# Optimization experiments

Hardware: AMD Instinct MI355X
Metric: run time of the kernel (lower is better)

The kernel has to match this reference:

```python
import jax, jax.numpy as jnp
import numpy as np


def setup_inputs() -> dict:
    key = jax.random.key(0)
    k1, k2 = jax.random.split(key)
    B, C, H, W = 16, 128, 128, 128
    x = jax.random.normal(k1, (B, C, H, W), dtype=jnp.float32)
    # 1x1 conv weight, no bias: [out_channels, in_channels]
    w = jax.random.normal(k2, (C, C), dtype=jnp.float32) * (1.0 / np.sqrt(C))
    return {"x": x, "w": w}


def reference(x, w):
    # x: [B, C, H, W]; original computes y = x @ (x^T x) / (H*W) over flattened
    # spatial dim N = H*W, then a 1x1 conv. We reassociate exactly:
    #   x @ (x^T x) == (x x^T) @ x   (associativity of matmul)
    # avoiding the O(N^2) intermediate; math is identical.
    B, C, H, W = x.shape
    N = H * W
    xf = x.reshape(B, C, N)                              # [B, C, N]
    gram = jnp.einsum('bcn,bdn->bcd', xf, xf) / N        # [B, C, C] = (x x^T)/N
    y = jnp.einsum('bcd,bdn->bcn', gram, xf)             # [B, C, N]
    y = y.reshape(B, C, H, W)
    # 1x1 conv (bias=False) == per-pixel channel mixing
    out = jnp.einsum('oc,bchw->bohw', w, y)              # [B, C, H, W]
    return out
```

## Files before the change

### kernel.cpp

```cpp
#include <hip/hip_runtime.h>

typedef __attribute__((ext_vector_type(8))) short bf16x8;
typedef __attribute__((ext_vector_type(4))) float f32x4;
typedef __attribute__((ext_vector_type(4))) float f4v;
typedef __attribute__((ext_vector_type(4))) unsigned short u16x4;

#define NB 16
#define NC 128
#define NN 16384
#define CHUNKS 32
#define KSTEPS 8

__device__ __forceinline__ unsigned int f2bf_pack(float lo, float hi) {
  unsigned int ulo = __float_as_uint(lo);
  unsigned int uhi = __float_as_uint(hi);
  ulo = (ulo + 0x7FFFu + ((ulo >> 16) & 1u)) >> 16;
  uhi = (uhi + 0x7FFFu + ((uhi >> 16) & 1u)) & 0xFFFF0000u;
  return ulo | uhi;
}

__device__ __forceinline__ unsigned short f2bf_one(float v) {
  unsigned int u = __float_as_uint(v);
  return (unsigned short)((u + 0x7FFFu + ((u >> 16) & 1u)) >> 16);
}

__device__ __forceinline__ float bf2f(unsigned short u) {
  return __uint_as_float(((unsigned int)u) << 16);
}

__global__ __launch_bounds__(256, 2)
void nlm_gram_kernel(const float* __restrict__ x, unsigned short* __restrict__ partials) {
  __shared__ __align__(16) char lds[2 * 128 * 64 * 2];
  const int t = threadIdx.x;
  const int g = blockIdx.x;
  const int b  = g / CHUNKS;
  const int ch = g % CHUNKS;
  const int lane = t & 63, wv = t >> 6, l15 = lane & 15, q = lane >> 4;

  const float* xb = x + (size_t)b * NC * NN + (size_t)ch * (KSTEPS * 64);

  f32x4 acc[2][8];
#pragma unroll
  for (int i = 0; i < 2; ++i)
#pragma unroll
    for (int j = 0; j < 8; ++j) acc[i][j] = (f32x4){0.f, 0.f, 0.f, 0.f};

  int srow[4], sseg[4];
#pragma unroll
  for (int i = 0; i < 4; ++i) { int id = t + 256 * i; srow[i] = id >> 3; sseg[i] = id & 7; }

  f4v pfA[4][2], pfB[4][2];

#define LOADPF(PF, KS)                                                      \
  {                                                                         \
    _Pragma("unroll") for (int i = 0; i < 4; ++i) {                         \
      const float* src = xb + (size_t)srow[i] * NN + (KS)*64 + sseg[i] * 8; \
      PF[i][0] = *(const f4v*)src;                                          \
      PF[i][1] = *(const f4v*)(src + 4);                                    \
    }                                                                       \
  }

#define PACKPF(PF, BUF)                                                     \
  {                                                                         \
    _Pragma("unroll") for (int i = 0; i < 4; ++i) {                         \
      uint4 pk;                                                             \
      pk.x = f2bf_pack(PF[i][0][0], PF[i][0][1]);                           \
      pk.y = f2bf_pack(PF[i][0][2], PF[i][0][3]);                           \
      pk.z = f2bf_pack(PF[i][1][0], PF[i][1][1]);                           \
      pk.w = f2bf_pack(PF[i][1][2], PF[i][1][3]);                           \
      int byte = (srow[i] * 128 + sseg[i] * 16) ^ ((srow[i] & 7) << 4);     \
      *(uint4*)((BUF) + byte) = pk;                                         \
    }                                                                       \
  }

#define MFMAPH(BUF)                                                                          \
  {                                                                                          \
    _Pragma("unroll") for (int kh = 0; kh < 2; ++kh) {                                       \
      const int kbyte = kh * 64 + q * 16;                                                    \
      int ra = wv * 32 + l15;                                                                \
      bf16x8 a0 = *(const bf16x8*)((BUF) + ((ra * 128 + kbyte) ^ ((ra & 7) << 4)));          \
      int rb = wv * 32 + 16 + l15;                                                           \
      bf16x8 a1 = *(const bf16x8*)((BUF) + ((rb * 128 + kbyte) ^ ((rb & 7) << 4)));          \
      _Pragma("unroll") for (int ct = 0; ct < 8; ++ct) {                                     \
        int rc = ct * 16 + l15;                                                              \
        bf16x8 bb = *(const bf16x8*)((BUF) + ((rc * 128 + kbyte) ^ ((rc & 7) << 4)));        \
        acc[0][ct] = __builtin_amdgcn_mfma_f32_16x16x32_bf16(a0, bb, acc[0][ct], 0, 0, 0);   \
        acc[1][ct] = __builtin_amdgcn_mfma_f32_16x16x32_bf16(a1, bb, acc[1][ct], 0, 0, 0);   \
      }                                                                                      \
    }                                                                                        \
  }

  char* buf0 = lds;
  char* buf1 = lds + 16384;

  LOADPF(pfA, 0);
  PACKPF(pfA, buf0);
  LOADPF(pfB, 1);
  __syncthreads();

#pragma unroll 1
  for (int ks = 0; ks < KSTEPS; ks += 2) {
    if (ks + 2 < KSTEPS) LOADPF(pfA, ks + 2);
    MFMAPH(buf0);
    if (ks + 1 < KSTEPS) PACKPF(pfB, buf1);
    __syncthreads();
    if (ks + 1 < KSTEPS) {
      if (ks + 3 < KSTEPS) LOADPF(pfB, ks + 3);
      MFMAPH(buf1);
      if (ks + 2 < KSTEPS) PACKPF(pfA, buf0);
      __syncthreads();
    }
  }

  unsigned short* lds16 = (unsigned short*)lds;
#pragma unroll
  for (int rt = 0; rt < 2; ++rt)
#pragma unroll
    for (int ct = 0; ct < 8; ++ct)
#pragma unroll
      for (int r = 0; r < 4; ++r) {
        int i = wv * 32 + rt * 16 + q * 4 + r;
        int j = ct * 16 + l15;
        lds16[i * 128 + j] = f2bf_one(acc[rt][ct][r]);
      }
  __syncthreads();

  unsigned short* part = partials + (size_t)g * (NC * NC);
#pragma unroll
  for (int ii = 0; ii < 8; ++ii) {
    int off = ii * 4096 + t * 16;
    *(uint4*)((char*)part + off) = *(const uint4*)(lds + off);
  }
#undef LOADPF
#undef PACKPF
#undef MFMAPH
}

__global__ __launch_bounds__(256)
void nlm_gramw_kernel(const unsigned short* __restrict__ partials, const float* __restrict__ w,
                      unsigned short* __restrict__ Mbf) {
  __shared__ __align__(16) float glds[8 * 128];
  const int t = threadIdx.x;
  const int b  = blockIdx.x >> 4;
  const int d0 = (blockIdx.x & 15) * 8;

  const int rr = t >> 5;
  const int c4 = (t & 31) * 4;
  const unsigned short* pb =
      partials + (size_t)b * CHUNKS * (NC * NC) + (d0 + rr) * 128 + c4;
  f4v s = (f4v){0.f, 0.f, 0.f, 0.f};
  for (int chn = 0; chn < CHUNKS; ++chn) {
    u16x4 v = *(const u16x4*)(pb + (size_t)chn * (NC * NC));
    s[0] += bf2f(v[0]);
    s[1] += bf2f(v[1]);
    s[2] += bf2f(v[2]);
    s[3] += bf2f(v[3]);
  }
  s *= (1.0f / 16384.0f);
  *(f4v*)(glds + rr * 128 + c4) = s;
  __syncthreads();

  const int o  = t & 127;
  const int j0 = (t >> 7) * 4;
  float m[4] = {0.f, 0.f, 0.f, 0.f};
  for (int c = 0; c < 128; c += 4) {
    f4v wr = *(const f4v*)(w + o * 128 + c);
#pragma unroll
    for (int j = 0; j < 4; ++j) {
      f4v gv = *(const f4v*)(glds + (j0 + j) * 128 + c);
      m[j] = fmaf(wr[0], gv[0], m[j]);
      m[j] = fmaf(wr[1], gv[1], m[j]);
      m[j] = fmaf(wr[2], gv[2], m[j]);
      m[j] = fmaf(wr[3], gv[3], m[j]);
    }
  }
  uint2 pk;
  pk.x = f2bf_pack(m[0], m[1]);
  pk.y = f2bf_pack(m[2], m[3]);
  *(uint2*)(Mbf + (size_t)b * NC * NC + o * 128 + d0 + j0) = pk;
}

__global__ __launch_bounds__(256, 2)
void nlm_out_kernel(const float* __restrict__ x, const unsigned short* __restrict__ Mbf,
                    float* __restrict__ out) {
  __shared__ __align__(16) char lds[128 * 128 * 2];
  const int t = threadIdx.x;
  const int b = (NB - 1) - (blockIdx.x >> 7);
  const int n0 = (blockIdx.x & 127) * 128;
  const int lane = t & 63, wv = t >> 6, l15 = lane & 15, q = lane >> 4;

  bf16x8 afr[2][4];
  const unsigned short* mb = Mbf + (size_t)b * NC * NC;
#pragma unroll
  for (int rt = 0; rt < 2; ++rt)
#pragma unroll
    for (int ks = 0; ks < 4; ++ks) {
      int o = wv * 32 + rt * 16 + l15;
      afr[rt][ks] = *(const bf16x8*)(mb + o * 128 + ks * 32 + q * 8);
    }

  const float* xb = x + (size_t)b * NC * NN + n0;
#pragma unroll
  for (int i = 0; i < 2; ++i) {
    int id = t + 256 * i;
    int nb = id & 31, cb = id >> 5;
    const float* src = xb + (size_t)(cb * 8) * NN + nb * 4;
    f4v v[8];
#pragma unroll
    for (int r = 0; r < 8; ++r) v[r] = *(const f4v*)(src + (size_t)r * NN);
#pragma unroll
    for (int j = 0; j < 4; ++j) {
      int n = nb * 4 + j;
      uint4 pk;
      pk.x = f2bf_pack(v[0][j], v[1][j]);
      pk.y = f2bf_pack(v[2][j], v[3][j]);
      pk.z = f2bf_pack(v[4][j], v[5][j]);
      pk.w = f2bf_pack(v[6][j], v[7][j]);
      int byte = (n * 256 + cb * 16) ^ ((((n & 7) ^ ((n >> 3) & 7))) << 4);
      *(uint4*)(lds + byte) = pk;
    }
  }
  __syncthreads();

  f32x4 acc[2][8];
#pragma unroll
  for (int i = 0; i < 2; ++i)
#pragma unroll
    for (int j = 0; j < 8; ++j) acc[i][j] = (f32x4){0.f, 0.f, 0.f, 0.f};

#pragma unroll
  for (int ks = 0; ks < 4; ++ks) {
#pragma unroll
    for (int ct = 0; ct < 8; ++ct) {
      int n = ct * 16 + l15;
      int byte = (n * 256 + ks * 64 + q * 16) ^ ((((n & 7) ^ ((n >> 3) & 7))) << 4);
      bf16x8 bfr = *(const bf16x8*)(lds + byte);
      acc[0][ct] = __builtin_amdgcn_mfma_f32_16x16x32_bf16(afr[0][ks], bfr, acc[0][ct], 0, 0, 0);
      acc[1][ct] = __builtin_amdgcn_mfma_f32_16x16x32_bf16(afr[1][ks], bfr, acc[1][ct], 0, 0, 0);
    }
  }

  float* ob = out + (size_t)b * NC * NN + n0;
#pragma unroll
  for (int rt = 0; rt < 2; ++rt)
#pragma unroll
    for (int ct = 0; ct < 8; ++ct)
#pragma unroll
      for (int r = 0; r < 4; ++r) {
        int o = wv * 32 + rt * 16 + q * 4 + r;
        int n = ct * 16 + l15;
        ob[(size_t)o * NN + n] = acc[rt][ct][r];
      }
}

extern "C" void kernel_launch(void* const* d_in, const int* in_sizes, int n_in,
                              void* d_out, int out_size, void* d_ws, size_t ws_size,
                              hipStream_t stream) {
  const float* x = (const float*)d_in[0];
  const float* w = (const float*)d_in[1];
  float* out = (float*)d_out;

  char* wsp = (char*)d_ws;
  unsigned short* partials = (unsigned short*)wsp;
  wsp += (size_t)NB * CHUNKS * NC * NC * 2;
  unsigned short* Mbf = (unsigned short*)wsp;

  hipLaunchKernelGGL(nlm_gram_kernel, dim3(NB * CHUNKS), dim3(256), 0, stream,
                     x, partials);
  hipLaunchKernelGGL(nlm_gramw_kernel, dim3(NB * 16), dim3(256), 0, stream,
                     partials, w, Mbf);
  hipLaunchKernelGGL(nlm_out_kernel, dim3(NB * 128), dim3(256), 0, stream,
                     x, Mbf, out);
}
```

Measured before the change: 81.14 us.

## Write bf16 copy of x in gram kernel and reuse it in output kernel

The gram kernel now stores the bf16-packed tiles it already computes into a workspace copy of x. The output kernel reads this half-size bf16 copy instead of re-reading and converting fp32 x. This halves the input bytes of the output kernel and removes its conversion work. In exchange, the gram kernel adds an equal amount of global writes, so total traffic is about the same unless the copy stays in cache.

New measurement: 93.47 us. +15.2%, slower.

```diff
diff --git a/kernel.cpp b/kernel.cpp
--- a/kernel.cpp
+++ b/kernel.cpp
@@ -29,7 +29,8 @@
 }
 
 __global__ __launch_bounds__(256, 2)
-void nlm_gram_kernel(const float* __restrict__ x, unsigned short* __restrict__ partials) {
+void nlm_gram_kernel(const float* __restrict__ x, unsigned short* __restrict__ partials,
+                     unsigned short* __restrict__ xbf) {
   __shared__ __align__(16) char lds[2 * 128 * 64 * 2];
   const int t = threadIdx.x;
   const int g = blockIdx.x;
@@ -60,7 +61,7 @@
     }                                                                       \
   }
 
-#define PACKPF(PF, BUF)                                                     \
+#define PACKPF(PF, BUF, KS)                                                 \
   {                                                                         \
     _Pragma("unroll") for (int i = 0; i < 4; ++i) {                         \
       uint4 pk;                                                             \
@@ -70,6 +71,8 @@
       pk.w = f2bf_pack(PF[i][1][2], PF[i][1][3]);                           \
       int byte = (srow[i] * 128 + sseg[i] * 16) ^ ((srow[i] & 7) << 4);     \
       *(uint4*)((BUF) + byte) = pk;                                         \
+      *(uint4*)(xbf + ((size_t)(b * NC + srow[i])) * NN +                   \
+                (size_t)ch * (KSTEPS * 64) + (KS)*64 + sseg[i] * 8) = pk;   \
     }                                                                       \
   }
 
@@ -94,7 +97,7 @@
   char* buf1 = lds + 16384;
 
   LOADPF(pfA, 0);
-  PACKPF(pfA, buf0);
+  PACKPF(pfA, buf0, 0);
   LOADPF(pfB, 1);
   __syncthreads();
 
@@ -102,12 +105,12 @@
   for (int ks = 0; ks < KSTEPS; ks += 2) {
     if (ks + 2 < KSTEPS) LOADPF(pfA, ks + 2);
     MFMAPH(buf0);
-    if (ks + 1 < KSTEPS) PACKPF(pfB, buf1);
+    if (ks + 1 < KSTEPS) PACKPF(pfB, buf1, ks + 1);
     __syncthreads();
     if (ks + 1 < KSTEPS) {
       if (ks + 3 < KSTEPS) LOADPF(pfB, ks + 3);
       MFMAPH(buf1);
-      if (ks + 2 < KSTEPS) PACKPF(pfA, buf0);
+      if (ks + 2 < KSTEPS) PACKPF(pfA, buf0, ks + 2);
       __syncthreads();
     }
   }
@@ -181,8 +184,8 @@
 }
 
 __global__ __launch_bounds__(256, 2)
-void nlm_out_kernel(const float* __restrict__ x, const unsigned short* __restrict__ Mbf,
-                    float* __restrict__ out) {
+void nlm_out_kernel(const unsigned short* __restrict__ xbf,
+                    const unsigned short* __restrict__ Mbf, float* __restrict__ out) {
   __shared__ __align__(16) char lds[128 * 128 * 2];
   const int t = threadIdx.x;
   const int b = (NB - 1) - (blockIdx.x >> 7);
@@ -199,25 +202,22 @@
       afr[rt][ks] = *(const bf16x8*)(mb + o * 128 + ks * 32 + q * 8);
     }
 
-  const float* xb = x + (size_t)b * NC * NN + n0;
-#pragma unroll
-  for (int i = 0; i < 2; ++i) {
-    int id = t + 256 * i;
-    int nb = id & 31, cb = id >> 5;
-    const float* src = xb + (size_t)(cb * 8) * NN + nb * 4;
-    f4v v[8];
-#pragma unroll
-    for (int r = 0; r < 8; ++r) v[r] = *(const f4v*)(src + (size_t)r * NN);
-#pragma unroll
-    for (int j = 0; j < 4; ++j) {
-      int n = nb * 4 + j;
-      uint4 pk;
-      pk.x = f2bf_pack(v[0][j], v[1][j]);
-      pk.y = f2bf_pack(v[2][j], v[3][j]);
-      pk.z = f2bf_pack(v[4][j], v[5][j]);
-      pk.w = f2bf_pack(v[6][j], v[7][j]);
-      int byte = (n * 256 + cb * 16) ^ ((((n & 7) ^ ((n >> 3) & 7))) << 4);
-      *(uint4*)(lds + byte) = pk;
+  {
+    const unsigned short* xb = xbf + (size_t)b * NC * NN + n0;
+    const int c8 = t >> 4;
+    const int n8 = t & 15;
+    union U8 { bf16x8 v; unsigned short u[8]; } vr[8];
+#pragma unroll
+    for (int r = 0; r < 8; ++r)
+      vr[r].v = *(const bf16x8*)(xb + (size_t)(c8 * 8 + r) * NN + n8 * 8);
+#pragma unroll
+    for (int j = 0; j < 8; ++j) {
+      int n = n8 * 8 + j;
+      union { uint4 q; unsigned short u[8]; } o;
+#pragma unroll
+      for (int r = 0; r < 8; ++r) o.u[r] = vr[r].u[j];
+      int byte = (n * 256 + c8 * 16) ^ ((((n & 7) ^ ((n >> 3) & 7))) << 4);
+      *(uint4*)(lds + byte) = o.q;
     }
   }
   __syncthreads();
@@ -264,11 +264,13 @@
   unsigned short* partials = (unsigned short*)wsp;
   wsp += (size_t)NB * CHUNKS * NC * NC * 2;
   unsigned short* Mbf = (unsigned short*)wsp;
+  wsp += (size_t)NB * NC * NC * 2;
+  unsigned short* xbf = (unsigned short*)wsp;
 
   hipLaunchKernelGGL(nlm_gram_kernel, dim3(NB * CHUNKS), dim3(256), 0, stream,
-                     x, partials);
+                     x, partials, xbf);
   hipLaunchKernelGGL(nlm_gramw_kernel, dim3(NB * 16), dim3(256), 0, stream,
                      partials, w, Mbf);
   hipLaunchKernelGGL(nlm_out_kernel, dim3(NB * 128), dim3(256), 0, stream,
-                     x, Mbf, out);
-}
+                     xbf, Mbf, out);
+}
```
